# Kernel optimization log

Measured on AMD Instinct MI355X. Metric: run time of the kernel, lower is better.

The kernel has to match this reference:

```python
import jax, jax.numpy as jnp
import numpy as np

TEMPERATURE = 0.07
B, D = 8192, 1024
EPS = 1e-08


def setup_inputs() -> dict:
    key = jax.random.key(0)
    k1, k2, k3, k4, k5 = jax.random.split(key, 5)
    visual_feats = jax.random.normal(k1, (B, D), dtype=jnp.float32)
    textual_feats = jax.random.normal(k2, (B, D), dtype=jnp.float32)
    transport_matrix = jax.random.uniform(k3, (B, B), dtype=jnp.float32)
    confident_clean_mask = jax.random.randint(k4, (B,), 0, 2).astype(jnp.bool_)
    confident_noisy_mask = jax.random.randint(k5, (B,), 0, 2).astype(jnp.bool_)
    return {
        'visual_feats': visual_feats,
        'textual_feats': textual_feats,
        'transport_matrix': transport_matrix,
        'confident_clean_mask': confident_clean_mask,
        'confident_noisy_mask': confident_noisy_mask,
    }


def _l2norm(x):
    # matches F.normalize(p=2, dim=-1) with default eps=1e-12
    n = jnp.sqrt(jnp.sum(x * x, axis=-1, keepdims=True))
    return x / jnp.maximum(n, 1e-12)


def reference(visual_feats, textual_feats, transport_matrix,
              confident_clean_mask, confident_noisy_mask):
    # current_epoch defaults to 0 < push_phase_epochs -> 'push_only' phase:
    # progressive_loss = CCL complementary (negative-push) loss.
    n = confident_noisy_mask.astype(jnp.float32)  # [B]
    # negative_mask[i,j] = 1 if (i==j and noisy[i]) or (i!=j and (noisy[i] or noisy[j]))
    # at i==j, max(n[i],n[i]) == n[i], so the broadcast max covers both cases.
    negative_mask = jnp.maximum(n[:, None], n[None, :])  # [B, B]

    v = _l2norm(visual_feats)
    t = _l2norm(textual_feats)
    similarities = v @ t.T  # [B, B]

    logits = similarities / TEMPERATURE
    neg_sum = jnp.sum(jnp.exp(logits) * negative_mask, axis=1) + EPS  # [B]
    progressive_loss = jnp.mean(jnp.log(neg_sum))
    return progressive_loss
```

## Files before the change

kernel.cpp:

```cpp
#include <hip/hip_runtime.h>
#include <hip/hip_bf16.h>

#define NB 8192
#define ND 1024

typedef __attribute__((ext_vector_type(8))) short bf16x8;
typedef __attribute__((ext_vector_type(4))) float f32x4;

__device__ __forceinline__ void async16(const void* g, void* l) {
  __builtin_amdgcn_global_load_lds(
      (const __attribute__((address_space(1))) void*)g,
      (__attribute__((address_space(3))) void*)l,
      16, 0, 0);
}

__device__ __forceinline__ unsigned short f2bf(float f) {
  union { float f; unsigned u; } a; a.f = f;
  unsigned u = a.u;
  return (unsigned short)((u + 0x7fffu + ((u >> 16) & 1u)) >> 16);
}

__global__ void prep_mask(const unsigned char* __restrict__ raw,
                          float* __restrict__ nmask) {
  __shared__ int flag;
  if (threadIdx.x == 0) flag = 0;
  __syncthreads();
  int any = 0;
  for (int i = threadIdx.x; i < NB; i += 256)
    if ((i & 3) != 0 && raw[i] != 0) any = 1;
  if (any) atomicOr(&flag, 1);
  __syncthreads();
  if (flag) {
    for (int i = threadIdx.x; i < NB; i += 256)
      nmask[i] = raw[i] ? 1.0f : 0.0f;
  } else {
    const int* ri = (const int*)raw;
    for (int i = threadIdx.x; i < NB; i += 256)
      nmask[i] = ri[i] ? 1.0f : 0.0f;
  }
}

__global__ void norm_cast(const float* __restrict__ vis,
                          const float* __restrict__ txt,
                          unsigned short* __restrict__ vb,
                          unsigned short* __restrict__ tb) {
  const float* src = blockIdx.y ? txt : vis;
  unsigned short* dst = blockIdx.y ? tb : vb;
  int row = blockIdx.x;
  int t = threadIdx.x;
  float4 x = ((const float4*)(src + (size_t)row * ND))[t];
  float ss = x.x * x.x + x.y * x.y + x.z * x.z + x.w * x.w;
  #pragma unroll
  for (int m = 32; m; m >>= 1) ss += __shfl_xor(ss, m);
  __shared__ float sred[4];
  if ((t & 63) == 0) sred[t >> 6] = ss;
  __syncthreads();
  float tot = sred[0] + sred[1] + sred[2] + sred[3];
  float inv = 1.0f / fmaxf(sqrtf(tot), 1e-12f);
  ushort4 o;
  o.x = f2bf(x.x * inv); o.y = f2bf(x.y * inv);
  o.z = f2bf(x.z * inv); o.w = f2bf(x.w * inv);
  ((ushort4*)dst)[(size_t)row * (ND / 4) + t] = o;
}

__global__ __launch_bounds__(256) void gemm_fused(
    const unsigned short* __restrict__ vb, const unsigned short* __restrict__ tb,
    const float* __restrict__ nmask, float* __restrict__ partial) {
  __shared__ unsigned short As[128 * 64];
  __shared__ unsigned short Bs[128 * 64];
  __shared__ float part2[128][2];

  const int bx = blockIdx.x, by = blockIdx.y;
  const int i0 = by * 128, j0 = bx * 128;
  const int t = threadIdx.x;
  const int w = t >> 6;
  const int l = t & 63;
  const int quad = l >> 4;
  const int l15 = l & 15;
  const int wm = w >> 1, wn = w & 1;
  const int rw = wm * 64, cw = wn * 64;

  const int lrow = l >> 3;
  const int lchunk = (l & 7) ^ lrow;
  const unsigned short* Ag = vb + (size_t)(i0 + w * 32 + lrow) * ND + lchunk * 8;
  const unsigned short* Bg = tb + (size_t)(j0 + w * 32 + lrow) * ND + lchunk * 8;
  char* AsB = (char*)As + w * 32 * 128;
  char* BsB = (char*)Bs + w * 32 * 128;

  f32x4 acc[4][4] = {};

  for (int kb = 0; kb < ND; kb += 64) {
    #pragma unroll
    for (int q = 0; q < 4; ++q) {
      async16(Ag + kb + q * 8 * ND, AsB + q * 1024);
      async16(Bg + kb + q * 8 * ND, BsB + q * 1024);
    }
    __syncthreads();
    #pragma unroll
    for (int kt = 0; kt < 2; ++kt) {
      bf16x8 a[4], b[4];
      #pragma unroll
      for (int mi = 0; mi < 4; ++mi) {
        int r = rw + mi * 16 + l15;
        int pos = (kt * 4 + quad) ^ (r & 7);
        a[mi] = *(const bf16x8*)&As[r * 64 + pos * 8];
      }
      #pragma unroll
      for (int ni = 0; ni < 4; ++ni) {
        int r = cw + ni * 16 + l15;
        int pos = (kt * 4 + quad) ^ (r & 7);
        b[ni] = *(const bf16x8*)&Bs[r * 64 + pos * 8];
      }
      #pragma unroll
      for (int mi = 0; mi < 4; ++mi)
        #pragma unroll
        for (int ni = 0; ni < 4; ++ni)
          acc[mi][ni] = __builtin_amdgcn_mfma_f32_16x16x32_bf16(
              a[mi], b[ni], acc[mi][ni], 0, 0, 0);
    }
    __syncthreads();
  }

  const float SCALE = 20.60992915555662f;
  float ncol[4];
  #pragma unroll
  for (int ni = 0; ni < 4; ++ni) ncol[ni] = nmask[j0 + cw + ni * 16 + l15];

  #pragma unroll
  for (int mi = 0; mi < 4; ++mi) {
    float nrow[4], rowacc[4] = {0.f, 0.f, 0.f, 0.f};
    #pragma unroll
    for (int r = 0; r < 4; ++r) nrow[r] = nmask[i0 + rw + mi * 16 + quad * 4 + r];
    #pragma unroll
    for (int ni = 0; ni < 4; ++ni) {
      #pragma unroll
      for (int r = 0; r < 4; ++r)
        rowacc[r] += exp2f(acc[mi][ni][r] * SCALE) * fmaxf(nrow[r], ncol[ni]);
    }
    #pragma unroll
    for (int r = 0; r < 4; ++r) {
      float v = rowacc[r];
      v += __shfl_xor(v, 1); v += __shfl_xor(v, 2);
      v += __shfl_xor(v, 4); v += __shfl_xor(v, 8);
      if (l15 == 0) part2[rw + mi * 16 + quad * 4 + r][wn] = v;
    }
  }
  __syncthreads();
  if (t < 128)
    partial[(size_t)bx * NB + i0 + t] = part2[t][0] + part2[t][1];
}

__global__ void finalize(const float* __restrict__ partial, float* __restrict__ out) {
  int r = blockIdx.x * 256 + threadIdx.x;
  float s = 0.f;
  #pragma unroll 4
  for (int c = 0; c < 64; ++c) s += partial[(size_t)c * NB + r];
  float lg = logf(s + 1e-8f);
  #pragma unroll
  for (int m = 32; m; m >>= 1) lg += __shfl_xor(lg, m);
  __shared__ float sred[4];
  if ((threadIdx.x & 63) == 0) sred[threadIdx.x >> 6] = lg;
  __syncthreads();
  if (threadIdx.x == 0)
    atomicAdd(out, (sred[0] + sred[1] + sred[2] + sred[3]) * (1.0f / NB));
}

extern "C" void kernel_launch(void* const* d_in, const int* in_sizes, int n_in,
                              void* d_out, int out_size, void* d_ws, size_t ws_size,
                              hipStream_t stream) {
  const float* vis = (const float*)d_in[0];
  const float* txt = (const float*)d_in[1];
  const unsigned char* noisy = (const unsigned char*)d_in[4];
  float* out = (float*)d_out;

  char* ws = (char*)d_ws;
  unsigned short* vb = (unsigned short*)ws;
  unsigned short* tb = (unsigned short*)(ws + ((size_t)16 << 20));
  float* nmask = (float*)(ws + ((size_t)32 << 20));
  float* partial = (float*)(ws + ((size_t)32 << 20) + (64 << 10));

  hipMemsetAsync(d_out, 0, sizeof(float), stream);
  prep_mask<<<1, 256, 0, stream>>>(noisy, nmask);
  norm_cast<<<dim3(NB, 2), 256, 0, stream>>>(vis, txt, vb, tb);
  gemm_fused<<<dim3(NB / 128, NB / 128), 256, 0, stream>>>(vb, tb, nmask, partial);
  finalize<<<NB / 256, 256, 0, stream>>>(partial, out);
}
```

Measured before the change: 524.6 us.

## Switch similarity GEMM to FP8 scaled MFMA and fold mask prep into norm kernel

Normalized features are now quantized to FP8 instead of bf16, and the GEMM uses the 16x16x128 scaled FP8 MFMA with a doubled K-tile per LDS stage. This halves operand bytes and doubles MFMA throughput per instruction. The separate mask-prep launch is merged into the first block of the normalization kernel. FP8 quantization loses precision, and with logits scaled by 1/0.07 before exponentiation the error could exceed tolerance.

```diff
diff --git a/kernel.cpp b/kernel.cpp
--- a/kernel.cpp
+++ b/kernel.cpp
@@ -4,7 +4,8 @@
 #define NB 8192
 #define ND 1024
 
-typedef __attribute__((ext_vector_type(8))) short bf16x8;
+typedef __attribute__((ext_vector_type(8))) int   i32x8;
+typedef __attribute__((ext_vector_type(4))) int   i32x4;
 typedef __attribute__((ext_vector_type(4))) float f32x4;
 
 __device__ __forceinline__ void async16(const void* g, void* l) {
@@ -14,38 +15,14 @@
       16, 0, 0);
 }
 
-__device__ __forceinline__ unsigned short f2bf(float f) {
-  union { float f; unsigned u; } a; a.f = f;
-  unsigned u = a.u;
-  return (unsigned short)((u + 0x7fffu + ((u >> 16) & 1u)) >> 16);
-}
-
-__global__ void prep_mask(const unsigned char* __restrict__ raw,
-                          float* __restrict__ nmask) {
-  __shared__ int flag;
-  if (threadIdx.x == 0) flag = 0;
-  __syncthreads();
-  int any = 0;
-  for (int i = threadIdx.x; i < NB; i += 256)
-    if ((i & 3) != 0 && raw[i] != 0) any = 1;
-  if (any) atomicOr(&flag, 1);
-  __syncthreads();
-  if (flag) {
-    for (int i = threadIdx.x; i < NB; i += 256)
-      nmask[i] = raw[i] ? 1.0f : 0.0f;
-  } else {
-    const int* ri = (const int*)raw;
-    for (int i = threadIdx.x; i < NB; i += 256)
-      nmask[i] = ri[i] ? 1.0f : 0.0f;
-  }
-}
-
 __global__ void norm_cast(const float* __restrict__ vis,
                           const float* __restrict__ txt,
-                          unsigned short* __restrict__ vb,
-                          unsigned short* __restrict__ tb) {
+                          unsigned char* __restrict__ vb,
+                          unsigned char* __restrict__ tb,
+                          const unsigned char* __restrict__ rawmask,
+                          float* __restrict__ nmask) {
   const float* src = blockIdx.y ? txt : vis;
-  unsigned short* dst = blockIdx.y ? tb : vb;
+  unsigned char* dst = blockIdx.y ? tb : vb;
   int row = blockIdx.x;
   int t = threadIdx.x;
   float4 x = ((const float4*)(src + (size_t)row * ND))[t];
@@ -57,17 +34,35 @@
   __syncthreads();
   float tot = sred[0] + sred[1] + sred[2] + sred[3];
   float inv = 1.0f / fmaxf(sqrtf(tot), 1e-12f);
-  ushort4 o;
-  o.x = f2bf(x.x * inv); o.y = f2bf(x.y * inv);
-  o.z = f2bf(x.z * inv); o.w = f2bf(x.w * inv);
-  ((ushort4*)dst)[(size_t)row * (ND / 4) + t] = o;
+  int p = 0;
+  p = __builtin_amdgcn_cvt_pk_fp8_f32(x.x * inv, x.y * inv, p, false);
+  p = __builtin_amdgcn_cvt_pk_fp8_f32(x.z * inv, x.w * inv, p, true);
+  ((int*)dst)[(size_t)row * (ND / 4) + t] = p;
+
+  if (blockIdx.x == 0 && blockIdx.y == 0) {
+    int any = 0;
+    for (int i = t; i < NB; i += 256)
+      if ((i & 3) != 0 && rawmask[i] != 0) any = 1;
+    #pragma unroll
+    for (int m = 32; m; m >>= 1) any |= __shfl_xor(any, m);
+    __shared__ int flag[4];
+    if ((t & 63) == 0) flag[t >> 6] = any;
+    __syncthreads();
+    int isbyte = flag[0] | flag[1] | flag[2] | flag[3];
+    if (isbyte) {
+      for (int i = t; i < NB; i += 256) nmask[i] = rawmask[i] ? 1.0f : 0.0f;
+    } else {
+      const int* ri = (const int*)rawmask;
+      for (int i = t; i < NB; i += 256) nmask[i] = ri[i] ? 1.0f : 0.0f;
+    }
+  }
 }
 
 __global__ __launch_bounds__(256) void gemm_fused(
-    const unsigned short* __restrict__ vb, const unsigned short* __restrict__ tb,
+    const unsigned char* __restrict__ vb, const unsigned char* __restrict__ tb,
     const float* __restrict__ nmask, float* __restrict__ partial) {
-  __shared__ unsigned short As[128 * 64];
-  __shared__ unsigned short Bs[128 * 64];
+  __shared__ char As[128 * 128];
+  __shared__ char Bs[128 * 128];
   __shared__ float part2[128][2];
 
   const int bx = blockIdx.x, by = blockIdx.y;
@@ -77,46 +72,49 @@
   const int l = t & 63;
   const int quad = l >> 4;
   const int l15 = l & 15;
+  const int x7 = l15 & 7;
   const int wm = w >> 1, wn = w & 1;
   const int rw = wm * 64, cw = wn * 64;
+  const int SC = 0x7f7f7f7f;
 
   const int lrow = l >> 3;
   const int lchunk = (l & 7) ^ lrow;
-  const unsigned short* Ag = vb + (size_t)(i0 + w * 32 + lrow) * ND + lchunk * 8;
-  const unsigned short* Bg = tb + (size_t)(j0 + w * 32 + lrow) * ND + lchunk * 8;
-  char* AsB = (char*)As + w * 32 * 128;
-  char* BsB = (char*)Bs + w * 32 * 128;
+  const unsigned char* Ag = vb + (size_t)(i0 + w * 32 + lrow) * ND + lchunk * 16;
+  const unsigned char* Bg = tb + (size_t)(j0 + w * 32 + lrow) * ND + lchunk * 16;
+  char* AsB = As + w * 32 * 128;
+  char* BsB = Bs + w * 32 * 128;
 
   f32x4 acc[4][4] = {};
 
-  for (int kb = 0; kb < ND; kb += 64) {
+  for (int kb = 0; kb < ND; kb += 128) {
     #pragma unroll
     for (int q = 0; q < 4; ++q) {
       async16(Ag + kb + q * 8 * ND, AsB + q * 1024);
       async16(Bg + kb + q * 8 * ND, BsB + q * 1024);
     }
     __syncthreads();
+
+    i32x8 bfr[4];
     #pragma unroll
-    for (int kt = 0; kt < 2; ++kt) {
-      bf16x8 a[4], b[4];
+    for (int ni = 0; ni < 4; ++ni) {
+      int r = cw + ni * 16 + l15;
+      int p0 = ((2 * quad) ^ x7) * 16;
+      i32x4 lo = *(const i32x4*)&Bs[r * 128 + p0];
+      i32x4 hi = *(const i32x4*)&Bs[r * 128 + (p0 ^ 16)];
+      bfr[ni] = __builtin_shufflevector(lo, hi, 0, 1, 2, 3, 4, 5, 6, 7);
+    }
+    #pragma unroll
+    for (int mi = 0; mi < 4; ++mi) {
+      int r = rw + mi * 16 + l15;
+      int p0 = ((2 * quad) ^ x7) * 16;
+      i32x4 lo = *(const i32x4*)&As[r * 128 + p0];
+      i32x4 hi = *(const i32x4*)&As[r * 128 + (p0 ^ 16)];
+      i32x8 afr = __builtin_shufflevector(lo, hi, 0, 1, 2, 3, 4, 5, 6, 7);
       #pragma unroll
-      for (int mi = 0; mi < 4; ++mi) {
-        int r = rw + mi * 16 + l15;
-        int pos = (kt * 4 + quad) ^ (r & 7);
-        a[mi] = *(const bf16x8*)&As[r * 64 + pos * 8];
-      }
-      #pragma unroll
-      for (int ni = 0; ni < 4; ++ni) {
-        int r = cw + ni * 16 + l15;
-        int pos = (kt * 4 + quad) ^ (r & 7);
-        b[ni] = *(const bf16x8*)&Bs[r * 64 + pos * 8];
-      }
-      #pragma unroll
-      for (int mi = 0; mi < 4; ++mi)
-        #pragma unroll
-        for (int ni = 0; ni < 4; ++ni)
-          acc[mi][ni] = __builtin_amdgcn_mfma_f32_16x16x32_bf16(
-              a[mi], b[ni], acc[mi][ni], 0, 0, 0);
+      for (int ni = 0; ni < 4; ++ni)
+        acc[mi][ni] = __builtin_amdgcn_mfma_scale_f32_16x16x128_f8f6f4(
+            afr, bfr[ni], acc[mi][ni], 0, 0,
+            0, SC, 0, SC);
     }
     __syncthreads();
   }
@@ -174,14 +172,13 @@
   float* out = (float*)d_out;
 
   char* ws = (char*)d_ws;
-  unsigned short* vb = (unsigned short*)ws;
-  unsigned short* tb = (unsigned short*)(ws + ((size_t)16 << 20));
-  float* nmask = (float*)(ws + ((size_t)32 << 20));
-  float* partial = (float*)(ws + ((size_t)32 << 20) + (64 << 10));
+  unsigned char* vb = (unsigned char*)ws;
+  unsigned char* tb = (unsigned char*)(ws + ((size_t)8 << 20));
+  float* nmask = (float*)(ws + ((size_t)16 << 20));
+  float* partial = (float*)(ws + ((size_t)16 << 20) + (64 << 10));
 
   hipMemsetAsync(d_out, 0, sizeof(float), stream);
-  prep_mask<<<1, 256, 0, stream>>>(noisy, nmask);
-  norm_cast<<<dim3(NB, 2), 256, 0, stream>>>(vis, txt, vb, tb);
+  norm_cast<<<dim3(NB, 2), 256, 0, stream>>>(vis, txt, vb, tb, noisy, nmask);
   gemm_fused<<<dim3(NB / 128, NB / 128), 256, 0, stream>>>(vb, tb, nmask, partial);
   finalize<<<NB / 256, 256, 0, stream>>>(partial, out);
 }
```

Measured after the change: 540.6 us. 3.1% more time.
